# Optimization experiments

Measured on AMD Instinct MI355X. Metric: run time of the kernel, lower is better.

## Reference

```python
import jax, jax.numpy as jnp
import numpy as np

N_NODES = 50000
BN_EPS = 1e-5


def sage_conv(x, src, dst, Wl, Wr, b):
    # mean-aggregate neighbor features: message from src -> dst
    msg = x[src]                                             # [E, Din]
    s = jax.ops.segment_sum(msg, dst, num_segments=N_NODES)  # [N, Din]
    cnt = jax.ops.segment_sum(jnp.ones((src.shape[0],), x.dtype), dst,
                              num_segments=N_NODES)          # [N]
    mean = s / jnp.maximum(cnt, 1.0)[:, None]
    # PyG SAGEConv: lin_l(aggregated) (+bias) + lin_r(self), root_weight=True
    return mean @ Wl + b + x @ Wr


def batch_norm(x, gamma, beta):
    mu = jnp.mean(x, axis=0)
    var = jnp.var(x, axis=0)
    return (x - mu) * jax.lax.rsqrt(var + BN_EPS) * gamma + beta


def setup_inputs() -> dict:
    key = jax.random.key(0)
    ks = jax.random.split(key, 16)
    D_IN, D_H, D_OUT = 128, 128, 64
    x = jax.random.normal(ks[0], (N_NODES, D_IN), dtype=jnp.float32)
    edge_index = jax.random.randint(ks[1], (2, 800000), 0, N_NODES, dtype=jnp.int32)

    def xavier(k, din, dout):
        lim = float(np.sqrt(6.0 / (din + dout)))
        return jax.random.uniform(k, (din, dout), jnp.float32, -lim, lim)

    return {
        "x": x, "edge_index": edge_index,
        "Wl0": xavier(ks[2], D_IN, D_H), "Wr0": xavier(ks[3], D_IN, D_H),
        "b0": jnp.zeros((D_H,), jnp.float32),
        "g0": jnp.ones((D_H,), jnp.float32), "be0": jnp.zeros((D_H,), jnp.float32),
        "Wl1": xavier(ks[4], D_H, D_H), "Wr1": xavier(ks[5], D_H, D_H),
        "b1": jnp.zeros((D_H,), jnp.float32),
        "g1": jnp.ones((D_H,), jnp.float32), "be1": jnp.zeros((D_H,), jnp.float32),
        "Wl2": xavier(ks[6], D_H, D_OUT), "Wr2": xavier(ks[7], D_H, D_OUT),
        "b2": jnp.zeros((D_OUT,), jnp.float32),
    }


def reference(x, edge_index, Wl0, Wr0, b0, g0, be0,
              Wl1, Wr1, b1, g1, be1, Wl2, Wr2, b2):
    src, dst = edge_index[0], edge_index[1]
    h = sage_conv(x, src, dst, Wl0, Wr0, b0)
    h = jax.nn.relu(batch_norm(h, g0, be0))
    h = sage_conv(h, src, dst, Wl1, Wr1, b1)
    h = jax.nn.relu(batch_norm(h, g1, be1))
    h = sage_conv(h, src, dst, Wl2, Wr2, b2)
    return jax.nn.log_softmax(h, axis=-1)
```

## Files before the change

### kernel.cpp

```cpp
#include <hip/hip_runtime.h>
#include <hip/hip_bf16.h>

#define D_IN 128
#define D_OUT 64
#define BN_EPS 1e-5f
#define NB_PART 512

typedef short short8 __attribute__((ext_vector_type(8)));
typedef float f32x4 __attribute__((ext_vector_type(4)));
typedef float f32x2 __attribute__((ext_vector_type(2)));
typedef unsigned int u32x4 __attribute__((ext_vector_type(4)));
typedef unsigned int u32x2 __attribute__((ext_vector_type(2)));
typedef unsigned short ushort_t;
typedef unsigned int uint_t;

__device__ __forceinline__ float bf16lo(uint_t v) { return __uint_as_float(v << 16); }
__device__ __forceinline__ float bf16hi(uint_t v) { return __uint_as_float(v & 0xffff0000u); }
__device__ __forceinline__ float bf2f(ushort_t u) { return __uint_as_float(((uint_t)u) << 16); }
__device__ __forceinline__ ushort_t f2bf(float f) {
    union { __hip_bfloat16 h; ushort_t u; } cv;
    cv.h = __float2bfloat16(f);
    return cv.u;
}
__device__ __forceinline__ f32x4 ntload4(const float* p) {
    return __builtin_nontemporal_load((const f32x4*)p);
}


__global__ void hist_kernel(const int* __restrict__ dst, int* __restrict__ cnt, int E) {
    int i = blockIdx.x * 256 + threadIdx.x;
    if (i < E) atomicAdd(&cnt[__builtin_nontemporal_load(&dst[i])], 1);
}

__global__ void scan_part_kernel(const int* __restrict__ cnt, int* __restrict__ bsum, int n) {
    int i = blockIdx.x * 256 + threadIdx.x;
    int v = (i < n) ? cnt[i] : 0;
#pragma unroll
    for (int off = 1; off < 64; off <<= 1) v += __shfl_xor(v, off);
    __shared__ int ws[4];
    int lane = threadIdx.x & 63, wid = threadIdx.x >> 6;
    if (lane == 0) ws[wid] = v;
    __syncthreads();
    if (threadIdx.x == 0) bsum[blockIdx.x] = ws[0] + ws[1] + ws[2] + ws[3];
}

__global__ void scan_mid_kernel(const int* __restrict__ bsum, int* __restrict__ bpre,
                                int* __restrict__ offs, int PB, int n) {
    int t = threadIdx.x;
    int v = (t < PB) ? bsum[t] : 0;
    int lane = t & 63, wid = t >> 6;
    int sc = v;
#pragma unroll
    for (int off = 1; off < 64; off <<= 1) {
        int u = __shfl_up(sc, off);
        if (lane >= off) sc += u;
    }
    __shared__ int ws[4];
    if (lane == 63) ws[wid] = sc;
    __syncthreads();
    int wb = 0;
    for (int w = 0; w < 4; w++) if (w < wid) wb += ws[w];
    int incl = sc + wb;
    if (t < PB) bpre[t] = incl - v;
    if (t == PB - 1) offs[n] = incl;
}

__global__ void scan_final_kernel(const int* __restrict__ cnt, const int* __restrict__ bpre,
                                  int* __restrict__ offs, int* __restrict__ cursor, int n) {
    int b = blockIdx.x, t = threadIdx.x;
    int i = b * 256 + t;
    int v = (i < n) ? cnt[i] : 0;
    int lane = t & 63, wid = t >> 6;
    int sc = v;
#pragma unroll
    for (int off = 1; off < 64; off <<= 1) {
        int u = __shfl_up(sc, off);
        if (lane >= off) sc += u;
    }
    __shared__ int ws[4];
    if (lane == 63) ws[wid] = sc;
    __syncthreads();
    int wb = 0;
    for (int w = 0; w < 4; w++) if (w < wid) wb += ws[w];
    if (i < n) {
        int e = bpre[b] + wb + sc - v;
        offs[i] = e;
        cursor[i] = e;
    }
}

__global__ void scatter_kernel(const int* __restrict__ src, const int* __restrict__ dst,
                               int* __restrict__ cursor, ushort_t* __restrict__ sorted_src,
                               int E, int passW) {
    int lo = blockIdx.y * passW, hi = lo + passW;
    int i = blockIdx.x * 256 + threadIdx.x;
    if (i < E) {
        int d = __builtin_nontemporal_load(&dst[i]);
        if (d >= lo && d < hi) {
            int s = __builtin_nontemporal_load(&src[i]);
            int p = atomicAdd(&cursor[d], 1);
            sorted_src[p] = (ushort_t)s;
        }
    }
}


__global__ void wswz_kernel(const float* __restrict__ Wl0, const float* __restrict__ Wr0,
                            const float* __restrict__ Wl1, const float* __restrict__ Wr1,
                            const float* __restrict__ Wl2, const float* __restrict__ Wr2,
                            short* __restrict__ o0l, short* __restrict__ o0r,
                            short* __restrict__ o1l, short* __restrict__ o1r,
                            short* __restrict__ o2l, short* __restrict__ o2r) {
    int layer = blockIdx.z;
    int Nn = (layer == 2) ? 64 : 128;
    const float* W;
    short* out;
    if (layer == 0) { W = blockIdx.y ? Wr0 : Wl0; out = blockIdx.y ? o0r : o0l; }
    else if (layer == 1) { W = blockIdx.y ? Wr1 : Wl1; out = blockIdx.y ? o1r : o1l; }
    else { W = blockIdx.y ? Wr2 : Wl2; out = blockIdx.y ? o2r : o2l; }
    int g = blockIdx.x * 256 + threadIdx.x;
    int nchunks = (Nn / 16) * 4;
    int chunk = g >> 6, lane = g & 63;
    if (chunk >= nchunks) return;
    int nf = chunk >> 2, kk = chunk & 3;
    short8 s;
#pragma unroll
    for (int j = 0; j < 8; j++) {
        float v = W[(size_t)(kk * 32 + (lane >> 4) * 8 + j) * Nn + nf * 16 + (lane & 15)];
        s[j] = (short)f2bf(v);
    }
    *(short8*)&out[((size_t)(chunk << 6) + lane) * 8] = s;
}


template <int TN, bool BF16IN>
__global__ __launch_bounds__(TN == 128 ? 256 : 128)
void gemm2_mfma(const void* __restrict__ Ain, const short* __restrict__ WlF,
                const short* __restrict__ WrF, ushort_t* __restrict__ Yb,
                ushort_t* __restrict__ Zb, const float* __restrict__ stats,
                const float* __restrict__ gamma, const float* __restrict__ beta, int M) {
    __shared__ short As[64 * 136];
    __shared__ float sc[128], sh[128];
    const int tid = threadIdx.x;
    const int lane = tid & 63;
    const int w = tid >> 6;
    const int row0 = blockIdx.x * 64;
    const int NT = (TN == 128) ? 256 : 128;

    if (BF16IN) {
        if (tid < 128) {
            float invM = 1.0f / (float)M;
            float mu = stats[tid] * invM;
            float var = stats[128 + tid] * invM - mu * mu;
            float scale = gamma[tid] * rsqrtf(var + BN_EPS);
            sc[tid] = scale;
            sh[tid] = beta[tid] - mu * scale;
        }
        __syncthreads();
    }

    for (int c = tid; c < 1024; c += NT) {
        int r = c >> 4, off = (c & 15) * 8;
        short8 v8 = {0, 0, 0, 0, 0, 0, 0, 0};
        if (row0 + r < M) {
            if (BF16IN) {
                const ushort_t* ap = (const ushort_t*)Ain + (size_t)(row0 + r) * 128 + off;
                short8 h = *(const short8*)ap;
#pragma unroll
                for (int j = 0; j < 8; j++) {
                    float f = bf2f((ushort_t)h[j]);
                    f = fmaxf(f * sc[off + j] + sh[off + j], 0.f);
                    v8[j] = (short)f2bf(f);
                }
            } else {
                const float* ap = (const float*)Ain + (size_t)(row0 + r) * 128 + off;
                f32x4 f0 = ntload4(ap);
                f32x4 f1 = ntload4(ap + 4);
#pragma unroll
                for (int j = 0; j < 4; j++) {
                    v8[j] = (short)f2bf(f0[j]);
                    v8[4 + j] = (short)f2bf(f1[j]);
                }
            }
        }
        *(short8*)&As[r * 136 + off] = v8;
    }
    __syncthreads();

    const short* WF;
    ushort_t* D;
    int col0;
    if (TN == 128) {
        bool isY = (w < 2);
        WF = isY ? WlF : WrF;
        D = isY ? Yb : Zb;
        col0 = (w & 1) * 64;
    } else {
        bool isY = (w == 0);
        WF = isY ? WlF : WrF;
        D = isY ? Yb : Zb;
        col0 = 0;
    }

    short8 a[4][4];
#pragma unroll
    for (int m = 0; m < 4; m++)
#pragma unroll
        for (int kk = 0; kk < 4; kk++)
            a[m][kk] = *(const short8*)&As[(m * 16 + (lane & 15)) * 136 + kk * 32 + (lane >> 4) * 8];

    f32x4 acc[4][4];
#pragma unroll
    for (int m = 0; m < 4; m++)
#pragma unroll
        for (int n = 0; n < 4; n++) acc[m][n] = (f32x4){0.f, 0.f, 0.f, 0.f};

#pragma unroll
    for (int kk = 0; kk < 4; kk++) {
#pragma unroll
        for (int n = 0; n < 4; n++) {
            short8 b = *(const short8*)&WF[(size_t)(((col0 >> 4) + n) * 4 + kk) * 512 + lane * 8];
#pragma unroll
            for (int m = 0; m < 4; m++)
                acc[m][n] = __builtin_amdgcn_mfma_f32_16x16x32_bf16(a[m][kk], b, acc[m][n], 0, 0, 0);
        }
    }

#pragma unroll
    for (int m = 0; m < 4; m++) {
#pragma unroll
        for (int i = 0; i < 4; i++) {
            int gr = row0 + m * 16 + (lane >> 4) * 4 + i;
            if (gr < M) {
#pragma unroll
                for (int n = 0; n < 4; n++)
                    D[(size_t)gr * TN + col0 + n * 16 + (lane & 15)] = f2bf(acc[m][n][i]);
            }
        }
    }
}


__global__ __launch_bounds__(256) void agg128_kernel(const ushort_t* __restrict__ Yb,
                                                     const int* __restrict__ offs,
                                                     const ushort_t* __restrict__ sorted_src,
                                                     const float* __restrict__ bias,
                                                     const ushort_t* __restrict__ Zb,
                                                     ushort_t* __restrict__ Hb, int N) {
    int wv = blockIdx.x * 4 + (threadIdx.x >> 6);
    int lane = threadIdx.x & 63;
    int half = lane >> 5, l = lane & 31;
    int node = wv * 2 + half;
    if (node >= N) return;
    int s0 = offs[node], s1 = offs[node + 1];
    float a0 = 0.f, a1 = 0.f, a2 = 0.f, a3 = 0.f;
    int k = s0;
    for (; k + 8 <= s1; k += 8) {
        int idx[8];
#pragma unroll
        for (int j = 0; j < 8; j++) idx[j] = __builtin_nontemporal_load(&sorted_src[k + j]);
        u32x2 v[8];
#pragma unroll
        for (int j = 0; j < 8; j++) v[j] = *(const u32x2*)&Yb[(size_t)idx[j] * 128 + l * 4];
#pragma unroll
        for (int j = 0; j < 8; j++) {
            a0 += bf16lo(v[j][0]);
            a1 += bf16hi(v[j][0]);
            a2 += bf16lo(v[j][1]);
            a3 += bf16hi(v[j][1]);
        }
    }
    if (k + 4 <= s1) {
        int idx[4];
#pragma unroll
        for (int j = 0; j < 4; j++) idx[j] = __builtin_nontemporal_load(&sorted_src[k + j]);
#pragma unroll
        for (int j = 0; j < 4; j++) {
            u32x2 v = *(const u32x2*)&Yb[(size_t)idx[j] * 128 + l * 4];
            a0 += bf16lo(v[0]);
            a1 += bf16hi(v[0]);
            a2 += bf16lo(v[1]);
            a3 += bf16hi(v[1]);
        }
        k += 4;
    }
    for (; k < s1; k++) {
        u32x2 v = *(const u32x2*)&Yb[(size_t)sorted_src[k] * 128 + l * 4];
        a0 += bf16lo(v[0]);
        a1 += bf16hi(v[0]);
        a2 += bf16lo(v[1]);
        a3 += bf16hi(v[1]);
    }
    float inv = 1.0f / fmaxf((float)(s1 - s0), 1.0f);
    float4 bb = *(const float4*)&bias[l * 4];
    u32x2 z = __builtin_nontemporal_load((const u32x2*)&Zb[(size_t)node * 128 + l * 4]);
    float h0 = bf16lo(z[0]) + a0 * inv + bb.x;
    float h1 = bf16hi(z[0]) + a1 * inv + bb.y;
    float h2 = bf16lo(z[1]) + a2 * inv + bb.z;
    float h3 = bf16hi(z[1]) + a3 * inv + bb.w;
    u32x2 o;
    o[0] = (uint_t)f2bf(h0) | ((uint_t)f2bf(h1) << 16);
    o[1] = (uint_t)f2bf(h2) | ((uint_t)f2bf(h3) << 16);
    __builtin_nontemporal_store(o, (u32x2*)&Hb[(size_t)node * 128 + l * 4]);
}


__global__ __launch_bounds__(256) void agg_lsm_kernel(const ushort_t* __restrict__ Yb,
                                                      const int* __restrict__ offs,
                                                      const ushort_t* __restrict__ sorted_src,
                                                      const float* __restrict__ bias,
                                                      const ushort_t* __restrict__ Zb,
                                                      float* __restrict__ out, int N) {
    int wv = blockIdx.x * 4 + (threadIdx.x >> 6);
    int lane = threadIdx.x & 63;
    int half = lane >> 5, l = lane & 31;
    int node = wv * 2 + half;
    if (node >= N) return;
    int s0 = offs[node], s1 = offs[node + 1];
    float a0 = 0.f, a1 = 0.f;
    int k = s0;
    for (; k + 4 <= s1; k += 4) {
        int idx[4];
#pragma unroll
        for (int j = 0; j < 4; j++) idx[j] = __builtin_nontemporal_load(&sorted_src[k + j]);
#pragma unroll
        for (int j = 0; j < 4; j++) {
            uint_t v = *(const uint_t*)&Yb[(size_t)idx[j] * 64 + l * 2];
            a0 += bf16lo(v);
            a1 += bf16hi(v);
        }
    }
    for (; k < s1; k++) {
        uint_t v = *(const uint_t*)&Yb[(size_t)sorted_src[k] * 64 + l * 2];
        a0 += bf16lo(v);
        a1 += bf16hi(v);
    }
    float inv = 1.0f / fmaxf((float)(s1 - s0), 1.0f);
    uint_t z = *(const uint_t*)&Zb[(size_t)node * 64 + l * 2];
    float2 bb = *(const float2*)&bias[l * 2];
    float v0 = bf16lo(z) + a0 * inv + bb.x;
    float v1 = bf16hi(z) + a1 * inv + bb.y;
    float m = fmaxf(v0, v1);
#pragma unroll
    for (int off = 16; off; off >>= 1) m = fmaxf(m, __shfl_xor(m, off));
    float s = expf(v0 - m) + expf(v1 - m);
#pragma unroll
    for (int off = 16; off; off >>= 1) s += __shfl_xor(s, off);
    float ls = logf(s);
    f32x2 o;
    o[0] = v0 - m - ls;
    o[1] = v1 - m - ls;
    __builtin_nontemporal_store(o, (f32x2*)&out[(size_t)node * 64 + l * 2]);
}


__global__ __launch_bounds__(256) void bn_part_kernel(const ushort_t* __restrict__ Hb,
                                                      float* __restrict__ P, int M) {
    int b = blockIdx.x;
    int R = (M + NB_PART - 1) / NB_PART;
    int r0 = b * R, r1 = min(r0 + R, M);
    int colg = (threadIdx.x & 15) * 8;
    int rowoff = threadIdx.x >> 4;
    float s[8], s2[8];
#pragma unroll
    for (int j = 0; j < 8; j++) { s[j] = 0.f; s2[j] = 0.f; }
    for (int r = r0 + rowoff; r < r1; r += 16) {
        u32x4 v = __builtin_nontemporal_load((const u32x4*)&Hb[(size_t)r * 128 + colg]);
#pragma unroll
        for (int q = 0; q < 4; q++) {
            float flo = bf16lo(v[q]);
            float fhi = bf16hi(v[q]);
            s[2 * q] += flo;
            s2[2 * q] += flo * flo;
            s[2 * q + 1] += fhi;
            s2[2 * q + 1] += fhi * fhi;
        }
    }
    __shared__ float ls[256][16];
#pragma unroll
    for (int j = 0; j < 8; j++) {
        ls[threadIdx.x][j] = s[j];
        ls[threadIdx.x][8 + j] = s2[j];
    }
    __syncthreads();
    if (threadIdx.x < 128) {
        int g = threadIdx.x >> 3, j = threadIdx.x & 7;
        float a = 0.f, c = 0.f;
#pragma unroll
        for (int kk = 0; kk < 16; kk++) {
            int id = kk * 16 + g;
            a += ls[id][j];
            c += ls[id][8 + j];
        }
        P[(size_t)b * 256 + threadIdx.x] = a;
        P[(size_t)b * 256 + 128 + threadIdx.x] = c;
    }
}

__global__ __launch_bounds__(1024) void bn_reduce_kernel(const float* __restrict__ P,
                                                         float* __restrict__ stats) {
    int c = threadIdx.x & 255, q = threadIdx.x >> 8;
    float acc = 0.f;
#pragma unroll 8
    for (int i = q * (NB_PART / 4); i < (q + 1) * (NB_PART / 4); i++)
        acc += P[(size_t)i * 256 + c];
    __shared__ float ls[4][256];
    ls[q][c] = acc;
    __syncthreads();
    if (threadIdx.x < 256) stats[c] = ls[0][c] + ls[1][c] + ls[2][c] + ls[3][c];
}


extern "C" void kernel_launch(void* const* d_in, const int* in_sizes, int n_in,
                              void* d_out, int out_size, void* d_ws, size_t ws_size,
                              hipStream_t stream) {
    const float* x   = (const float*)d_in[0];
    const int*   ei  = (const int*)d_in[1];
    const float* Wl0 = (const float*)d_in[2];
    const float* Wr0 = (const float*)d_in[3];
    const float* b0  = (const float*)d_in[4];
    const float* g0  = (const float*)d_in[5];
    const float* be0 = (const float*)d_in[6];
    const float* Wl1 = (const float*)d_in[7];
    const float* Wr1 = (const float*)d_in[8];
    const float* b1  = (const float*)d_in[9];
    const float* g1  = (const float*)d_in[10];
    const float* be1 = (const float*)d_in[11];
    const float* Wl2 = (const float*)d_in[12];
    const float* Wr2 = (const float*)d_in[13];
    const float* b2  = (const float*)d_in[14];

    const int N = in_sizes[0] / D_IN;
    const int E = in_sizes[1] / 2;
    const int PB = (N + 255) / 256;

    ushort_t* Hb = (ushort_t*)d_ws;
    ushort_t* Zb = Hb + (size_t)N * D_IN;
    ushort_t* Yb = Zb + (size_t)N * D_IN;
    int* cnt    = (int*)(Yb + (size_t)N * D_IN);
    int* offs   = cnt + N;
    int* cursor = offs + N + 1;
    int* bsum   = cursor + N;
    int* bpre   = bsum + 256;
    ushort_t* sorted = (ushort_t*)(bpre + 256);
    float* stats = (float*)(sorted + E + (E & 1));
    float* P = stats + 512;
    short* WlF0 = (short*)(P + NB_PART * 256);
    short* WrF0 = WlF0 + 16384;
    short* WlF1 = WrF0 + 16384;
    short* WrF1 = WlF1 + 16384;
    short* WlF2 = WrF1 + 16384;
    short* WrF2 = WlF2 + 8192;

    const int eb = (E + 255) / 256;

    hipMemsetAsync(cnt, 0, (size_t)N * sizeof(int), stream);
    hist_kernel<<<eb, 256, 0, stream>>>(ei + E, cnt, E);
    scan_part_kernel<<<PB, 256, 0, stream>>>(cnt, bsum, N);
    scan_mid_kernel<<<1, 256, 0, stream>>>(bsum, bpre, offs, PB, N);
    scan_final_kernel<<<PB, 256, 0, stream>>>(cnt, bpre, offs, cursor, N);
    scatter_kernel<<<dim3(eb, 2), 256, 0, stream>>>(ei, ei + E, cursor, sorted, E, (N + 1) / 2);

    wswz_kernel<<<dim3(8, 2, 3), 256, 0, stream>>>(Wl0, Wr0, Wl1, Wr1, Wl2, Wr2,
                                                   WlF0, WrF0, WlF1, WrF1, WlF2, WrF2);

    const int gb = (N + 63) / 64;
    const int ab = (N + 7) / 8;

    gemm2_mfma<128, false><<<gb, 256, 0, stream>>>(x, WlF0, WrF0, Yb, Zb,
                                                   nullptr, nullptr, nullptr, N);
    agg128_kernel<<<ab, 256, 0, stream>>>(Yb, offs, sorted, b0, Zb, Hb, N);
    bn_part_kernel<<<NB_PART, 256, 0, stream>>>(Hb, P, N);
    bn_reduce_kernel<<<1, 1024, 0, stream>>>(P, stats);

    gemm2_mfma<128, true><<<gb, 256, 0, stream>>>(Hb, WlF1, WrF1, Yb, Zb,
                                                  stats, g0, be0, N);
    agg128_kernel<<<ab, 256, 0, stream>>>(Yb, offs, sorted, b1, Zb, Hb, N);
    bn_part_kernel<<<NB_PART, 256, 0, stream>>>(Hb, P, N);
    bn_reduce_kernel<<<1, 1024, 0, stream>>>(P, stats + 256);

    gemm2_mfma<64, true><<<gb, 128, 0, stream>>>(Hb, WlF2, WrF2, Yb, Zb,
                                                 stats + 256, g1, be1, N);
    agg_lsm_kernel<<<ab, 256, 0, stream>>>(Yb, offs, sorted, b2, Zb, (float*)d_out, N);
}
```

Baseline: 347.5 us.

## Merge scan into single-block kernel, fold count zeroing into weight swizzle, unroll gathers

```diff
diff --git a/kernel.cpp b/kernel.cpp
--- a/kernel.cpp
+++ b/kernel.cpp
@@ -32,61 +32,48 @@
     if (i < E) atomicAdd(&cnt[__builtin_nontemporal_load(&dst[i])], 1);
 }
 
-__global__ void scan_part_kernel(const int* __restrict__ cnt, int* __restrict__ bsum, int n) {
-    int i = blockIdx.x * 256 + threadIdx.x;
-    int v = (i < n) ? cnt[i] : 0;
-#pragma unroll
-    for (int off = 1; off < 64; off <<= 1) v += __shfl_xor(v, off);
-    __shared__ int ws[4];
-    int lane = threadIdx.x & 63, wid = threadIdx.x >> 6;
-    if (lane == 0) ws[wid] = v;
+__global__ __launch_bounds__(1024) void scan_kernel(const int* __restrict__ cnt,
+                                                    int* __restrict__ offs,
+                                                    int* __restrict__ cursor, int n) {
+    __shared__ int wsum[16];
+    __shared__ int carry_s;
+    int tid = threadIdx.x;
+    int lane = tid & 63, wid = tid >> 6;
+    if (tid == 0) carry_s = 0;
     __syncthreads();
-    if (threadIdx.x == 0) bsum[blockIdx.x] = ws[0] + ws[1] + ws[2] + ws[3];
-}
-
-__global__ void scan_mid_kernel(const int* __restrict__ bsum, int* __restrict__ bpre,
-                                int* __restrict__ offs, int PB, int n) {
-    int t = threadIdx.x;
-    int v = (t < PB) ? bsum[t] : 0;
-    int lane = t & 63, wid = t >> 6;
-    int sc = v;
-#pragma unroll
-    for (int off = 1; off < 64; off <<= 1) {
-        int u = __shfl_up(sc, off);
-        if (lane >= off) sc += u;
-    }
-    __shared__ int ws[4];
-    if (lane == 63) ws[wid] = sc;
-    __syncthreads();
-    int wb = 0;
-    for (int w = 0; w < 4; w++) if (w < wid) wb += ws[w];
-    int incl = sc + wb;
-    if (t < PB) bpre[t] = incl - v;
-    if (t == PB - 1) offs[n] = incl;
-}
-
-__global__ void scan_final_kernel(const int* __restrict__ cnt, const int* __restrict__ bpre,
-                                  int* __restrict__ offs, int* __restrict__ cursor, int n) {
-    int b = blockIdx.x, t = threadIdx.x;
-    int i = b * 256 + t;
-    int v = (i < n) ? cnt[i] : 0;
-    int lane = t & 63, wid = t >> 6;
-    int sc = v;
-#pragma unroll
-    for (int off = 1; off < 64; off <<= 1) {
-        int u = __shfl_up(sc, off);
-        if (lane >= off) sc += u;
-    }
-    __shared__ int ws[4];
-    if (lane == 63) ws[wid] = sc;
-    __syncthreads();
-    int wb = 0;
-    for (int w = 0; w < 4; w++) if (w < wid) wb += ws[w];
-    if (i < n) {
-        int e = bpre[b] + wb + sc - v;
-        offs[i] = e;
-        cursor[i] = e;
-    }
+    const int CH = 4096;
+    for (int base = 0; base < n; base += CH) {
+        int i0 = base + tid * 4;
+        int v[4];
+#pragma unroll
+        for (int j = 0; j < 4; j++) { int i = i0 + j; v[j] = (i < n) ? cnt[i] : 0; }
+        int tsum = v[0] + v[1] + v[2] + v[3];
+        int sc = tsum;
+#pragma unroll
+        for (int off = 1; off < 64; off <<= 1) {
+            int t = __shfl_up(sc, off);
+            if (lane >= off) sc += t;
+        }
+        if (lane == 63) wsum[wid] = sc;
+        __syncthreads();
+        int wbase = 0;
+        for (int w = 0; w < 16; w++) if (w < wid) wbase += wsum[w];
+        int carry = carry_s;
+        __syncthreads();
+        int run = carry + wbase + sc - tsum;
+#pragma unroll
+        for (int j = 0; j < 4; j++) {
+            int i = i0 + j;
+            if (i < n) {
+                offs[i] = run;
+                cursor[i] = run;
+            }
+            run += v[j];
+        }
+        if (tid == 1023) carry_s = carry + wbase + sc;
+        __syncthreads();
+    }
+    if (tid == 0) offs[n] = carry_s;
 }
 
 __global__ void scatter_kernel(const int* __restrict__ src, const int* __restrict__ dst,
@@ -110,7 +97,11 @@
                             const float* __restrict__ Wl2, const float* __restrict__ Wr2,
                             short* __restrict__ o0l, short* __restrict__ o0r,
                             short* __restrict__ o1l, short* __restrict__ o1r,
-                            short* __restrict__ o2l, short* __restrict__ o2r) {
+                            short* __restrict__ o2l, short* __restrict__ o2r,
+                            int* __restrict__ cnt, int N) {
+    int fb = blockIdx.x + 8 * (blockIdx.y + 2 * blockIdx.z);
+    for (int i = fb * 256 + threadIdx.x; i < N; i += 48 * 256) cnt[i] = 0;
+
     int layer = blockIdx.z;
     int Nn = (layer == 2) ? 64 : 128;
     const float* W;
@@ -255,22 +246,22 @@
     int s0 = offs[node], s1 = offs[node + 1];
     float a0 = 0.f, a1 = 0.f, a2 = 0.f, a3 = 0.f;
     int k = s0;
-    for (; k + 8 <= s1; k += 8) {
-        int idx[8];
-#pragma unroll
-        for (int j = 0; j < 8; j++) idx[j] = __builtin_nontemporal_load(&sorted_src[k + j]);
-        u32x2 v[8];
-#pragma unroll
-        for (int j = 0; j < 8; j++) v[j] = *(const u32x2*)&Yb[(size_t)idx[j] * 128 + l * 4];
-#pragma unroll
-        for (int j = 0; j < 8; j++) {
+    for (; k + 16 <= s1; k += 16) {
+        int idx[16];
+#pragma unroll
+        for (int j = 0; j < 16; j++) idx[j] = __builtin_nontemporal_load(&sorted_src[k + j]);
+        u32x2 v[16];
+#pragma unroll
+        for (int j = 0; j < 16; j++) v[j] = *(const u32x2*)&Yb[(size_t)idx[j] * 128 + l * 4];
+#pragma unroll
+        for (int j = 0; j < 16; j++) {
             a0 += bf16lo(v[j][0]);
             a1 += bf16hi(v[j][0]);
             a2 += bf16lo(v[j][1]);
             a3 += bf16hi(v[j][1]);
         }
     }
-    if (k + 4 <= s1) {
+    for (; k + 4 <= s1; k += 4) {
         int idx[4];
 #pragma unroll
         for (int j = 0; j < 4; j++) idx[j] = __builtin_nontemporal_load(&sorted_src[k + j]);
@@ -282,7 +273,6 @@
             a2 += bf16lo(v[1]);
             a3 += bf16hi(v[1]);
         }
-        k += 4;
     }
     for (; k < s1; k++) {
         u32x2 v = *(const u32x2*)&Yb[(size_t)sorted_src[k] * 128 + l * 4];
@@ -319,6 +309,19 @@
     int s0 = offs[node], s1 = offs[node + 1];
     float a0 = 0.f, a1 = 0.f;
     int k = s0;
+    for (; k + 8 <= s1; k += 8) {
+        int idx[8];
+#pragma unroll
+        for (int j = 0; j < 8; j++) idx[j] = __builtin_nontemporal_load(&sorted_src[k + j]);
+        uint_t v[8];
+#pragma unroll
+        for (int j = 0; j < 8; j++) v[j] = *(const uint_t*)&Yb[(size_t)idx[j] * 64 + l * 2];
+#pragma unroll
+        for (int j = 0; j < 8; j++) {
+            a0 += bf16lo(v[j]);
+            a1 += bf16hi(v[j]);
+        }
+    }
     for (; k + 4 <= s1; k += 4) {
         int idx[4];
 #pragma unroll
@@ -432,7 +435,6 @@
 
     const int N = in_sizes[0] / D_IN;
     const int E = in_sizes[1] / 2;
-    const int PB = (N + 255) / 256;
 
     ushort_t* Hb = (ushort_t*)d_ws;
     ushort_t* Zb = Hb + (size_t)N * D_IN;
@@ -440,9 +442,7 @@
     int* cnt    = (int*)(Yb + (size_t)N * D_IN);
     int* offs   = cnt + N;
     int* cursor = offs + N + 1;
-    int* bsum   = cursor + N;
-    int* bpre   = bsum + 256;
-    ushort_t* sorted = (ushort_t*)(bpre + 256);
+    ushort_t* sorted = (ushort_t*)(cursor + N);
     float* stats = (float*)(sorted + E + (E & 1));
     float* P = stats + 512;
     short* WlF0 = (short*)(P + NB_PART * 256);
@@ -454,15 +454,13 @@
 
     const int eb = (E + 255) / 256;
 
-    hipMemsetAsync(cnt, 0, (size_t)N * sizeof(int), stream);
+    wswz_kernel<<<dim3(8, 2, 3), 256, 0, stream>>>(Wl0, Wr0, Wl1, Wr1, Wl2, Wr2,
+                                                   WlF0, WrF0, WlF1, WrF1, WlF2, WrF2,
+                                                   cnt, N);
+
     hist_kernel<<<eb, 256, 0, stream>>>(ei + E, cnt, E);
-    scan_part_kernel<<<PB, 256, 0, stream>>>(cnt, bsum, N);
-    scan_mid_kernel<<<1, 256, 0, stream>>>(bsum, bpre, offs, PB, N);
-    scan_final_kernel<<<PB, 256, 0, stream>>>(cnt, bpre, offs, cursor, N);
+    scan_kernel<<<1, 1024, 0, stream>>>(cnt, offs, cursor, N);
     scatter_kernel<<<dim3(eb, 2), 256, 0, stream>>>(ei, ei + E, cursor, sorted, E, (N + 1) / 2);
-
-    wswz_kernel<<<dim3(8, 2, 3), 256, 0, stream>>>(Wl0, Wr0, Wl1, Wr1, Wl2, Wr2,
-                                                   WlF0, WrF0, WlF1, WrF1, WlF2, WrF2);
 
     const int gb = (N + 63) / 64;
     const int ab = (N + 7) / 8;
```

New measurement: 383.3 us. 10.3% more time.
